# Kernel optimization log

Hardware: AMD Instinct MI355X
Metric: run time of the kernel (lower is better)

## Reference

```python
import jax, jax.numpy as jnp
import numpy as np

M, K = 8192, 4096
N_INT4, N_INT8 = 8192, 2816
N_TOTAL = N_INT4 + N_INT8


def setup_inputs() -> dict:
    key = jax.random.key(0)
    k1, k2, k3, k4, k5 = jax.random.split(key, 5)
    x = jax.random.normal(k1, (M, K), dtype=jnp.float32)
    # Precomputed dequantized weight buffers (what forward() actually consumes).
    # Scaled down ~1/sqrt(K) to keep activations O(1), mimicking dequantized int4/int8 weights.
    w_int4_deq = jax.random.normal(k2, (N_INT4, K), dtype=jnp.float32) * 0.02
    w_int8_deq = jax.random.normal(k3, (N_INT8, K), dtype=jnp.float32) * 0.02
    # inv_perm: random permutation mapping concatenated [int4|int8] channels back to original order
    inv_perm = jax.random.permutation(k4, N_TOTAL).astype(jnp.int64)
    bias = jax.random.normal(k5, (N_TOTAL,), dtype=jnp.float32)
    return {"x": x, "w_int4_deq": w_int4_deq, "w_int8_deq": w_int8_deq,
            "inv_perm": inv_perm, "bias": bias}


def reference(x, w_int4_deq, w_int8_deq, inv_perm, bias):
    # Two GEMMs on dequantized weight groups: y = x @ W^T
    y_int4 = jnp.einsum('mk,nk->mn', x, w_int4_deq)   # [M, N_int4]
    y_int8 = jnp.einsum('mk,nk->mn', x, w_int8_deq)   # [M, N_int8]
    y = jnp.concatenate([y_int4, y_int8], axis=-1)    # [M, N_total]
    # Output-channel permutation back to original layout, then bias add
    y = jnp.take(y, inv_perm, axis=-1) + bias
    return y
```

## Files before the change

kernel.cpp:

```cpp
#include <hip/hip_runtime.h>
#include <hip/hip_bf16.h>

#define M_DIM 8192
#define K_DIM 4096
#define N4    8192
#define N8    2816
#define NT    11008
#define TM    (M_DIM / 256)
#define TN    (NT / 256)
#define NKT   (K_DIM / 64)
#define NFULL 1280
#define GRID  1472

typedef __attribute__((ext_vector_type(4))) float  f32x4;
typedef __attribute__((ext_vector_type(4))) float  float4v;
typedef __attribute__((ext_vector_type(8))) __bf16 bf16x8;
typedef __attribute__((ext_vector_type(4))) unsigned short ushort4v;
typedef __attribute__((ext_vector_type(8))) unsigned short ushort8v;

__device__ __forceinline__ unsigned short f2bf(float f) {
  union { float f; unsigned int u; } v; v.f = f;
  unsigned int u = v.u;
  unsigned int r = u + 0x7FFFu + ((u >> 16) & 1u);
  return (unsigned short)(r >> 16);
}

__global__ void conv_x_kernel(const float* __restrict__ x,
                              unsigned short* __restrict__ xb, int n8) {
  int idx = blockIdx.x * blockDim.x + threadIdx.x;
  int stride = gridDim.x * blockDim.x;
  for (int i = idx; i < n8; i += stride) {
    const float4v* src = (const float4v*)(x + (size_t)i * 8);
    float4v a = src[0], b = src[1];
    ushort8v o;
    o[0] = f2bf(a[0]); o[1] = f2bf(a[1]); o[2] = f2bf(a[2]); o[3] = f2bf(a[3]);
    o[4] = f2bf(b[0]); o[5] = f2bf(b[1]); o[6] = f2bf(b[2]); o[7] = f2bf(b[3]);
    ((ushort8v*)xb)[i] = o;
  }
}

__global__ void conv_w_kernel(const float* __restrict__ w4,
                              const float* __restrict__ w8,
                              const int* __restrict__ inv_perm,
                              unsigned short* __restrict__ wb) {
  int j = blockIdx.x;
  int c = inv_perm[j];
  const float* src = (c < N4) ? (w4 + (size_t)c * K_DIM)
                              : (w8 + (size_t)(c - N4) * K_DIM);
  unsigned short* dst = wb + (size_t)j * K_DIM;
  int t = threadIdx.x;
#pragma unroll
  for (int it = 0; it < 4; ++it) {
    int e = it * 1024 + t * 4;
    float4v a = *(const float4v*)(src + e);
    ushort4v o;
    o[0] = f2bf(a[0]); o[1] = f2bf(a[1]); o[2] = f2bf(a[2]); o[3] = f2bf(a[3]);
    *(ushort4v*)(dst + e) = o;
  }
}

__global__ __launch_bounds__(512, 2)
void gemm256_kernel(const unsigned short* __restrict__ A,
                    const unsigned short* __restrict__ B,
                    const float* __restrict__ bias,
                    float* __restrict__ C) {
  __shared__ __align__(16) unsigned short lds[4 * 16384];

  int bid = blockIdx.x;
  int vbid, mhalf, is_half;
  if (bid < NFULL) { vbid = bid; mhalf = 0; is_half = 0; }
  else { int h = bid - NFULL; vbid = NFULL + (h >> 1); mhalf = h & 1; is_half = 1; }
  int wgid = (vbid & 7) * ((TM * TN) / 8) + (vbid >> 3);
  int tile_m = wgid / TN;
  int tile_n = wgid % TN;

  const int tid  = threadIdx.x;
  const int wid  = tid >> 6;
  const int lane = tid & 63;
  const int wr  = wid >> 2;
  const int wcn = wid & 3;
  const int l15 = lane & 15;
  const int rswz  = (lane & 7) << 4;
  const int coff0 = (((lane >> 4) * 16) + 0)  ^ rswz;
  const int coff1 = (((lane >> 4) * 16) + 64) ^ rswz;
  const int st_row8 = lane >> 3;
  const int st_scol = ((lane & 7) * 16) ^ ((lane & 0x38) << 1);

  const size_t brow0 = (size_t)tile_n * 256;

  auto stage = [&](const unsigned short* __restrict__ g, size_t grow0,
                   unsigned short* ltile, int q, int ktelem) {
    int row = q * 64 + wid * 8 + st_row8;
    const unsigned short* src =
        g + (grow0 + (size_t)row) * K_DIM + ktelem + (st_scol >> 1);
    unsigned short* dst = ltile + (q * 64 + wid * 8) * 64;
    __builtin_amdgcn_global_load_lds(
        (const __attribute__((address_space(1))) void*)src,
        (__attribute__((address_space(3))) void*)dst, 16, 0, 0);
  };
  auto fragld = [&](const unsigned short* ltile, int row, int coff) -> bf16x8 {
    return *(const bf16x8*)((const char*)ltile + row * 128 + coff);
  };

  if (is_half) {
    const size_t arowh = (size_t)tile_m * 256 + (size_t)mhalf * 128;
    f32x4 acch[4][4];
#pragma unroll
    for (int i = 0; i < 4; ++i)
#pragma unroll
      for (int j = 0; j < 4; ++j) acch[i][j] = (f32x4){0.f, 0.f, 0.f, 0.f};

    stage(A, arowh, lds + 0, 0, 0);      stage(A, arowh, lds + 0, 1, 0);
    stage(B, brow0, lds + 16384, 0, 0);  stage(B, brow0, lds + 16384, 1, 0);
    stage(B, brow0, lds + 16384, 2, 0);  stage(B, brow0, lds + 16384, 3, 0);
    asm volatile("s_waitcnt vmcnt(0)" ::: "memory");
    __builtin_amdgcn_s_barrier();

#pragma unroll 1
    for (int u = 0; u < NKT; ++u) {
      unsigned short* Ac = lds + (u & 1) * 32768;
      unsigned short* Bc = Ac + 16384;
      unsigned short* An = lds + (32768 - (u & 1) * 32768);
      if (u + 1 < NKT) {
        int kn = (u + 1) * 64;
        stage(A, arowh, An, 0, kn);      stage(A, arowh, An, 1, kn);
        stage(B, brow0, An + 16384, 0, kn); stage(B, brow0, An + 16384, 1, kn);
        stage(B, brow0, An + 16384, 2, kn); stage(B, brow0, An + 16384, 3, kn);
      }
      bf16x8 ah[4][2], bh[4][2];
#pragma unroll
      for (int m = 0; m < 4; ++m) {
        int row = wr * 64 + m * 16 + l15;
        ah[m][0] = fragld(Ac, row, coff0);
        ah[m][1] = fragld(Ac, row, coff1);
      }
#pragma unroll
      for (int n = 0; n < 4; ++n) {
        int row = wcn * 64 + n * 16 + l15;
        bh[n][0] = fragld(Bc, row, coff0);
        bh[n][1] = fragld(Bc, row, coff1);
      }
      asm volatile("s_waitcnt lgkmcnt(0)" ::: "memory");
      __builtin_amdgcn_sched_barrier(0);
      __builtin_amdgcn_s_setprio(1);
#pragma unroll
      for (int m = 0; m < 4; ++m)
#pragma unroll
        for (int n = 0; n < 4; ++n) {
          acch[m][n] = __builtin_amdgcn_mfma_f32_16x16x32_bf16(ah[m][0], bh[n][0], acch[m][n], 0, 0, 0);
          acch[m][n] = __builtin_amdgcn_mfma_f32_16x16x32_bf16(ah[m][1], bh[n][1], acch[m][n], 0, 0, 0);
        }
      __builtin_amdgcn_s_setprio(0);
      asm volatile("s_waitcnt vmcnt(0)" ::: "memory");
      __builtin_amdgcn_s_barrier();
    }

#pragma unroll
    for (int n = 0; n < 4; ++n) {
      int col = tile_n * 256 + wcn * 64 + n * 16 + l15;
      float bv = bias[col];
#pragma unroll
      for (int m = 0; m < 4; ++m) {
        int row0 = tile_m * 256 + mhalf * 128 + wr * 64 + m * 16 + ((lane >> 4) * 4);
#pragma unroll
        for (int r = 0; r < 4; ++r) {
          C[(size_t)(row0 + r) * NT + col] = acch[m][n][r] + bv;
        }
      }
    }
    return;
  }

  const size_t arow0 = (size_t)tile_m * 256;

  f32x4 acc[8][4];
#pragma unroll
  for (int i = 0; i < 8; ++i)
#pragma unroll
    for (int j = 0; j < 4; ++j) acc[i][j] = (f32x4){0.f, 0.f, 0.f, 0.f};

  bf16x8 b0[2][2];

  stage(A, arow0, lds + 0,     0, 0);  stage(A, arow0, lds + 0,     2, 0);
  stage(A, arow0, lds + 0,     1, 0);  stage(A, arow0, lds + 0,     3, 0);
  stage(B, brow0, lds + 16384, 0, 0);  stage(B, brow0, lds + 16384, 1, 0);
  stage(B, brow0, lds + 16384, 2, 0);  stage(B, brow0, lds + 16384, 3, 0);
  stage(A, arow0, lds + 32768, 0, 64); stage(A, arow0, lds + 32768, 2, 64);
  stage(B, brow0, lds + 49152, 0, 64); stage(B, brow0, lds + 49152, 1, 64);
  stage(B, brow0, lds + 49152, 2, 64); stage(B, brow0, lds + 49152, 3, 64);
  asm volatile("s_waitcnt vmcnt(6)" ::: "memory");
  __builtin_amdgcn_s_barrier();

#pragma unroll
  for (int n = 0; n < 2; ++n) {
    int row = wcn * 64 + n * 16 + l15;
    b0[n][0] = fragld(lds + 16384, row, coff0);
    b0[n][1] = fragld(lds + 16384, row, coff1);
  }

#define KITER(AC, BC, AN, UN1, UN2)                                           \
  {                                                                           \
    unsigned short* const Ac = (AC);                                          \
    unsigned short* const Bc = (BC);                                          \
    unsigned short* const An = (AN);                                          \
    const int un1 = (UN1);                                                    \
    const int un2 = (UN2);                                                    \
    bf16x8 a0[4][2], a1[4][2], b1[2][2];                                      \
                \
    _Pragma("unroll")                                                         \
    for (int m = 0; m < 4; ++m) {                                             \
      int row = wr * 128 + m * 16 + l15;                                      \
      a0[m][0] = fragld(Ac, row, coff0);                                      \
      a0[m][1] = fragld(Ac, row, coff1);                                      \
    }                                                                         \
    stage(A, arow0, An, 1, un1);                                              \
    stage(A, arow0, An, 3, un1);                                              \
    __builtin_amdgcn_s_barrier();                                             \
    asm volatile("s_waitcnt lgkmcnt(0)" ::: "memory");                        \
    __builtin_amdgcn_sched_barrier(0);                                        \
    __builtin_amdgcn_s_setprio(1);                                            \
    _Pragma("unroll")                                                         \
    for (int m = 0; m < 4; ++m)                                               \
      _Pragma("unroll")                                                       \
      for (int n = 0; n < 2; ++n) {                                           \
        acc[m][n] = __builtin_amdgcn_mfma_f32_16x16x32_bf16(a0[m][0], b0[n][0], acc[m][n], 0, 0, 0); \
        acc[m][n] = __builtin_amdgcn_mfma_f32_16x16x32_bf16(a0[m][1], b0[n][1], acc[m][n], 0, 0, 0); \
      }                                                                       \
    __builtin_amdgcn_s_setprio(0);                                            \
    __builtin_amdgcn_s_barrier();                                             \
     \
    _Pragma("unroll")                                                         \
    for (int n = 0; n < 2; ++n) {                                             \
      int row = wcn * 64 + (2 + n) * 16 + l15;                                \
      b1[n][0] = fragld(Bc, row, coff0);                                      \
      b1[n][1] = fragld(Bc, row, coff1);                                      \
    }                                                                         \
    stage(A, arow0, Ac, 0, un2);                                              \
    stage(A, arow0, Ac, 2, un2);                                              \
    __builtin_amdgcn_s_barrier();                                             \
    asm volatile("s_waitcnt lgkmcnt(0)" ::: "memory");                        \
    __builtin_amdgcn_sched_barrier(0);                                        \
    __builtin_amdgcn_s_setprio(1);                                            \
    _Pragma("unroll")                                                         \
    for (int m = 0; m < 4; ++m)                                               \
      _Pragma("unroll")                                                       \
      for (int n = 0; n < 2; ++n) {                                           \
        acc[m][2 + n] = __builtin_amdgcn_mfma_f32_16x16x32_bf16(a0[m][0], b1[n][0], acc[m][2 + n], 0, 0, 0); \
        acc[m][2 + n] = __builtin_amdgcn_mfma_f32_16x16x32_bf16(a0[m][1], b1[n][1], acc[m][2 + n], 0, 0, 0); \
      }                                                                       \
    __builtin_amdgcn_s_setprio(0);                                            \
    asm volatile("s_waitcnt vmcnt(10)" ::: "memory");      \
    __builtin_amdgcn_s_barrier();                                             \
            \
    _Pragma("unroll")                                                         \
    for (int m = 0; m < 4; ++m) {                                             \
      int row = wr * 128 + 64 + m * 16 + l15;                                 \
      a1[m][0] = fragld(Ac, row, coff0);                                      \
      a1[m][1] = fragld(Ac, row, coff1);                                      \
    }                                                                         \
    stage(B, brow0, Bc, 0, un2);                                              \
    stage(B, brow0, Bc, 1, un2);                                              \
    __builtin_amdgcn_s_barrier();                                             \
    asm volatile("s_waitcnt lgkmcnt(0)" ::: "memory");                        \
    __builtin_amdgcn_sched_barrier(0);                                        \
    __builtin_amdgcn_s_setprio(1);                                            \
    _Pragma("unroll")                                                         \
    for (int m = 0; m < 4; ++m)                                               \
      _Pragma("unroll")                                                       \
      for (int n = 0; n < 2; ++n) {                                           \
        acc[4 + m][n] = __builtin_amdgcn_mfma_f32_16x16x32_bf16(a1[m][0], b0[n][0], acc[4 + m][n], 0, 0, 0); \
        acc[4 + m][n] = __builtin_amdgcn_mfma_f32_16x16x32_bf16(a1[m][1], b0[n][1], acc[4 + m][n], 0, 0, 0); \
      }                                                                       \
    __builtin_amdgcn_s_setprio(0);                                            \
    __builtin_amdgcn_s_barrier();                                             \
                             \
    stage(B, brow0, Bc, 2, un2);                                              \
    stage(B, brow0, Bc, 3, un2);                                              \
    asm volatile("s_waitcnt vmcnt(8)" ::: "memory");                          \
    __builtin_amdgcn_s_barrier();                                             \
    _Pragma("unroll")                                                         \
    for (int n = 0; n < 2; ++n) {                                             \
      int row = wcn * 64 + n * 16 + l15;                                      \
      b0[n][0] = fragld(An + 16384, row, coff0);                              \
      b0[n][1] = fragld(An + 16384, row, coff1);                              \
    }                                                                         \
    __builtin_amdgcn_s_setprio(1);                                            \
    _Pragma("unroll")                                                         \
    for (int m = 0; m < 4; ++m)                                               \
      _Pragma("unroll")                                                       \
      for (int n = 0; n < 2; ++n) {                                           \
        acc[4 + m][2 + n] = __builtin_amdgcn_mfma_f32_16x16x32_bf16(a1[m][0], b1[n][0], acc[4 + m][2 + n], 0, 0, 0); \
        acc[4 + m][2 + n] = __builtin_amdgcn_mfma_f32_16x16x32_bf16(a1[m][1], b1[n][1], acc[4 + m][2 + n], 0, 0, 0); \
      }                                                                       \
    __builtin_amdgcn_s_setprio(0);                                            \
    __builtin_amdgcn_s_barrier();                                             \
  }

#pragma unroll 1
  for (int u = 0; u < NKT; u += 2) {
    const int k1 = ((u + 1 < NKT) ? (u + 1) : (NKT - 1)) * 64;
    const int k2 = ((u + 2 < NKT) ? (u + 2) : (NKT - 1)) * 64;
    const int k3 = ((u + 3 < NKT) ? (u + 3) : (NKT - 1)) * 64;
    KITER(lds + 0,     lds + 16384, lds + 32768, k1, k2);
    KITER(lds + 32768, lds + 49152, lds + 0,     k2, k3);
  }
#undef KITER

#pragma unroll
  for (int n = 0; n < 4; ++n) {
    int col = tile_n * 256 + wcn * 64 + n * 16 + l15;
    float bv = bias[col];
#pragma unroll
    for (int m = 0; m < 8; ++m) {
      int row0 = tile_m * 256 + wr * 128 + m * 16 + ((lane >> 4) * 4);
#pragma unroll
      for (int r = 0; r < 4; ++r) {
        C[(size_t)(row0 + r) * NT + col] = acc[m][n][r] + bv;
      }
    }
  }
}

__global__ void gemm_fused_f32_kernel(const float* __restrict__ x,
                                      const float* __restrict__ w4,
                                      const float* __restrict__ w8,
                                      const int* __restrict__ inv_perm,
                                      const float* __restrict__ bias,
                                      float* __restrict__ C) {
  __shared__ __align__(16) unsigned short Alds[128 * 64];
  __shared__ __align__(16) unsigned short Blds[128 * 64];

  int bid = blockIdx.x;
  int wgid = (bid & 7) * ((M_DIM / 128) * (NT / 128) / 8) + (bid >> 3);
  int tile_n = wgid % (NT / 128);
  int tile_m = wgid / (NT / 128);

  const int tid  = threadIdx.x;
  const int wid  = tid >> 6;
  const int lane = tid & 63;
  const int wr = wid >> 1, wc = wid & 1;

  f32x4 acc[4][4];
#pragma unroll
  for (int i = 0; i < 4; ++i)
#pragma unroll
    for (int j = 0; j < 4; ++j) acc[i][j] = (f32x4){0.f, 0.f, 0.f, 0.f};

  const int lrow = lane >> 3;
  const int lcol = (lane & 7) * 8;

  const float* asrc[4];
  const float* bsrc[4];
  int ldsoff[4];
#pragma unroll
  for (int s = 0; s < 4; ++s) {
    int rb = s * 32 + wid * 8 + lrow;
    asrc[s] = x + (size_t)(tile_m * 128 + rb) * K_DIM + lcol;
    int c = inv_perm[tile_n * 128 + rb];
    bsrc[s] = ((c < N4) ? (w4 + (size_t)c * K_DIM)
                        : (w8 + (size_t)(c - N4) * K_DIM)) + lcol;
    ldsoff[s] = rb * 64 + lcol;
  }

  for (int kt = 0; kt < K_DIM; kt += 64) {
#pragma unroll
    for (int s = 0; s < 4; ++s) {
      float4v a0 = *(const float4v*)(asrc[s] + kt);
      float4v a1 = *(const float4v*)(asrc[s] + kt + 4);
      float4v b0 = *(const float4v*)(bsrc[s] + kt);
      float4v b1 = *(const float4v*)(bsrc[s] + kt + 4);
      ushort8v oa, ob;
      oa[0]=f2bf(a0[0]); oa[1]=f2bf(a0[1]); oa[2]=f2bf(a0[2]); oa[3]=f2bf(a0[3]);
      oa[4]=f2bf(a1[0]); oa[5]=f2bf(a1[1]); oa[6]=f2bf(a1[2]); oa[7]=f2bf(a1[3]);
      ob[0]=f2bf(b0[0]); ob[1]=f2bf(b0[1]); ob[2]=f2bf(b0[2]); ob[3]=f2bf(b0[3]);
      ob[4]=f2bf(b1[0]); ob[5]=f2bf(b1[1]); ob[6]=f2bf(b1[2]); ob[7]=f2bf(b1[3]);
      *(ushort8v*)&Alds[ldsoff[s]] = oa;
      *(ushort8v*)&Blds[ldsoff[s]] = ob;
    }
    __syncthreads();

#pragma unroll
    for (int kk = 0; kk < 2; ++kk) {
      bf16x8 af[4], bfr[4];
#pragma unroll
      for (int i = 0; i < 4; ++i) {
        int row = wr * 64 + i * 16 + (lane & 15);
        af[i] = *(const bf16x8*)&Alds[row * 64 + kk * 32 + (lane >> 4) * 8];
      }
#pragma unroll
      for (int j = 0; j < 4; ++j) {
        int row = wc * 64 + j * 16 + (lane & 15);
        bfr[j] = *(const bf16x8*)&Blds[row * 64 + kk * 32 + (lane >> 4) * 8];
      }
#pragma unroll
      for (int i = 0; i < 4; ++i)
#pragma unroll
        for (int j = 0; j < 4; ++j)
          acc[i][j] = __builtin_amdgcn_mfma_f32_16x16x32_bf16(af[i], bfr[j], acc[i][j], 0, 0, 0);
    }
    __syncthreads();
  }

#pragma unroll
  for (int j = 0; j < 4; ++j) {
    int col = tile_n * 128 + wc * 64 + j * 16 + (lane & 15);
    float bv = bias[col];
#pragma unroll
    for (int i = 0; i < 4; ++i) {
      int row0 = tile_m * 128 + wr * 64 + i * 16 + ((lane >> 4) * 4);
#pragma unroll
      for (int r = 0; r < 4; ++r) {
        C[(size_t)(row0 + r) * NT + col] = acc[i][j][r] + bv;
      }
    }
  }
}

extern "C" void kernel_launch(void* const* d_in, const int* in_sizes, int n_in,
                              void* d_out, int out_size, void* d_ws, size_t ws_size,
                              hipStream_t stream) {
  const float* x    = (const float*)d_in[0];
  const float* w4   = (const float*)d_in[1];
  const float* w8   = (const float*)d_in[2];
  const int*   perm = (const int*)d_in[3];
  const float* bias = (const float*)d_in[4];
  float*       out  = (float*)d_out;

  const size_t xb_bytes = (size_t)M_DIM * K_DIM * 2;
  const size_t wb_bytes = (size_t)NT * K_DIM * 2;

  if (ws_size >= xb_bytes + wb_bytes) {
    unsigned short* xb = (unsigned short*)d_ws;
    unsigned short* wb = xb + (size_t)M_DIM * K_DIM;
    conv_x_kernel<<<2048, 256, 0, stream>>>(x, xb, (M_DIM * K_DIM) / 8);
    conv_w_kernel<<<NT, 256, 0, stream>>>(w4, w8, perm, wb);
    gemm256_kernel<<<GRID, 512, 0, stream>>>(xb, wb, bias, out);
  } else {
    int grid = (M_DIM / 128) * (NT / 128);
    gemm_fused_f32_kernel<<<grid, 256, 0, stream>>>(x, w4, w8, perm, bias, out);
  }
}
```

Measured before the change: 731.2 us.

## Pre-swizzle weights into MFMA fragment layout and load B directly to registers

The weight conversion kernel now writes bf16 weights in a per-wave MFMA fragment order, so the GEMM can load B fragments straight from global memory into registers instead of staging them through LDS. LDS usage is halved (only A is staged), and the main-loop pipeline is simplified to one A-tile prefetch per k-step with fewer barriers. The aim is to cut LDS traffic and barrier overhead and possibly raise occupancy. The cost is that B is re-read from global/L2 by each wave without LDS sharing, and global-load latency is exposed within the k-step.

```diff
diff --git a/kernel.cpp b/kernel.cpp
--- a/kernel.cpp
+++ b/kernel.cpp
@@ -39,32 +39,46 @@
   }
 }
 
-__global__ void conv_w_kernel(const float* __restrict__ w4,
-                              const float* __restrict__ w8,
-                              const int* __restrict__ inv_perm,
-                              unsigned short* __restrict__ wb) {
-  int j = blockIdx.x;
-  int c = inv_perm[j];
-  const float* src = (c < N4) ? (w4 + (size_t)c * K_DIM)
-                              : (w8 + (size_t)(c - N4) * K_DIM);
-  unsigned short* dst = wb + (size_t)j * K_DIM;
-  int t = threadIdx.x;
-#pragma unroll
-  for (int it = 0; it < 4; ++it) {
-    int e = it * 1024 + t * 4;
-    float4v a = *(const float4v*)(src + e);
-    ushort4v o;
-    o[0] = f2bf(a[0]); o[1] = f2bf(a[1]); o[2] = f2bf(a[2]); o[3] = f2bf(a[3]);
-    *(ushort4v*)(dst + e) = o;
+__global__ void conv_w2_kernel(const float* __restrict__ w4,
+                               const float* __restrict__ w8,
+                               const int* __restrict__ inv_perm,
+                               unsigned short* __restrict__ w2) {
+  int task = blockIdx.x * 4 + (threadIdx.x >> 6);
+  int lane = threadIdx.x & 63;
+  int rg = task >> 4;
+  int uq = task & 15;
+  int r  = rg * 16 + (lane & 15);
+  int u  = uq * 4 + (lane >> 4);
+  int pr = inv_perm[r];
+  const float* src = (pr < N4) ? (w4 + (size_t)pr * K_DIM)
+                               : (w8 + (size_t)(pr - N4) * K_DIM);
+  float4v v[16];
+#pragma unroll
+  for (int i = 0; i < 16; ++i) v[i] = *(const float4v*)(src + u * 64 + i * 4);
+
+  const int T = rg >> 2;
+  const int n = rg & 3;
+  const size_t cbase = (((size_t)T * 64 + u) * 8 + n * 2) * 64 + (lane & 15);
+#pragma unroll
+  for (int kk = 0; kk < 2; ++kk) {
+#pragma unroll
+    for (int g = 0; g < 4; ++g) {
+      float4v lo = v[kk * 8 + g * 2], hi = v[kk * 8 + g * 2 + 1];
+      ushort8v o;
+      o[0] = f2bf(lo[0]); o[1] = f2bf(lo[1]); o[2] = f2bf(lo[2]); o[3] = f2bf(lo[3]);
+      o[4] = f2bf(hi[0]); o[5] = f2bf(hi[1]); o[6] = f2bf(hi[2]); o[7] = f2bf(hi[3]);
+      size_t ci = cbase + (size_t)kk * 64 + (g << 4);
+      *(ushort8v*)(w2 + ci * 8) = o;
+    }
   }
 }
 
 __global__ __launch_bounds__(512, 2)
 void gemm256_kernel(const unsigned short* __restrict__ A,
-                    const unsigned short* __restrict__ B,
+                    const unsigned short* __restrict__ Bw2,
                     const float* __restrict__ bias,
                     float* __restrict__ C) {
-  __shared__ __align__(16) unsigned short lds[4 * 16384];
+  __shared__ __align__(16) unsigned short lds[2 * 16384];
 
   int bid = blockIdx.x;
   int vbid, mhalf, is_half;
@@ -85,60 +99,54 @@
   const int coff1 = (((lane >> 4) * 16) + 64) ^ rswz;
   const int st_row8 = lane >> 3;
   const int st_scol = ((lane & 7) * 16) ^ ((lane & 0x38) << 1);
-
-  const size_t brow0 = (size_t)tile_n * 256;
-
-  auto stage = [&](const unsigned short* __restrict__ g, size_t grow0,
+  const int dstoff  = wid * 512;
+
+  const unsigned short* w2lane =
+      Bw2 + ((size_t)(tile_n * 4 + wcn) * 32768 + (size_t)lane) * 8;
+
+  auto stage = [&](const unsigned short* __restrict__ srcb,
                    unsigned short* ltile, int q, int ktelem) {
-    int row = q * 64 + wid * 8 + st_row8;
-    const unsigned short* src =
-        g + (grow0 + (size_t)row) * K_DIM + ktelem + (st_scol >> 1);
-    unsigned short* dst = ltile + (q * 64 + wid * 8) * 64;
     __builtin_amdgcn_global_load_lds(
-        (const __attribute__((address_space(1))) void*)src,
-        (__attribute__((address_space(3))) void*)dst, 16, 0, 0);
+        (const __attribute__((address_space(1))) void*)(srcb + q * (64 * K_DIM) + ktelem),
+        (__attribute__((address_space(3))) void*)(ltile + q * 4096 + dstoff), 16, 0, 0);
   };
   auto fragld = [&](const unsigned short* ltile, int row, int coff) -> bf16x8 {
     return *(const bf16x8*)((const char*)ltile + row * 128 + coff);
   };
 
   if (is_half) {
-    const size_t arowh = (size_t)tile_m * 256 + (size_t)mhalf * 128;
+    const unsigned short* aSh =
+        A + ((size_t)tile_m * 256 + (size_t)mhalf * 128 + (size_t)(wid * 8 + st_row8)) * K_DIM
+          + (st_scol >> 1);
     f32x4 acch[4][4];
 #pragma unroll
     for (int i = 0; i < 4; ++i)
 #pragma unroll
       for (int j = 0; j < 4; ++j) acch[i][j] = (f32x4){0.f, 0.f, 0.f, 0.f};
 
-    stage(A, arowh, lds + 0, 0, 0);      stage(A, arowh, lds + 0, 1, 0);
-    stage(B, brow0, lds + 16384, 0, 0);  stage(B, brow0, lds + 16384, 1, 0);
-    stage(B, brow0, lds + 16384, 2, 0);  stage(B, brow0, lds + 16384, 3, 0);
+    stage(aSh, lds + 0, 0, 0); stage(aSh, lds + 0, 1, 0);
     asm volatile("s_waitcnt vmcnt(0)" ::: "memory");
     __builtin_amdgcn_s_barrier();
 
 #pragma unroll 1
     for (int u = 0; u < NKT; ++u) {
-      unsigned short* Ac = lds + (u & 1) * 32768;
-      unsigned short* Bc = Ac + 16384;
-      unsigned short* An = lds + (32768 - (u & 1) * 32768);
-      if (u + 1 < NKT) {
-        int kn = (u + 1) * 64;
-        stage(A, arowh, An, 0, kn);      stage(A, arowh, An, 1, kn);
-        stage(B, brow0, An + 16384, 0, kn); stage(B, brow0, An + 16384, 1, kn);
-        stage(B, brow0, An + 16384, 2, kn); stage(B, brow0, An + 16384, 3, kn);
-      }
-      bf16x8 ah[4][2], bh[4][2];
+      unsigned short* Ac = lds + (u & 1) * 8192;
+      unsigned short* An = lds + (8192 - (u & 1) * 8192);
+      const unsigned short* wB = w2lane + (size_t)u * 4096;
+      bf16x8 bh[4][2];
+#pragma unroll
+      for (int n = 0; n < 4; ++n) {
+        bh[n][0] = *(const bf16x8*)(wB + (n * 2) * 512);
+        bh[n][1] = *(const bf16x8*)(wB + (n * 2 + 1) * 512);
+      }
+      int kn = ((u + 1 < NKT) ? (u + 1) : (NKT - 1)) * 64;
+      stage(aSh, An, 0, kn); stage(aSh, An, 1, kn);
+      bf16x8 ah[4][2];
 #pragma unroll
       for (int m = 0; m < 4; ++m) {
         int row = wr * 64 + m * 16 + l15;
         ah[m][0] = fragld(Ac, row, coff0);
         ah[m][1] = fragld(Ac, row, coff1);
-      }
-#pragma unroll
-      for (int n = 0; n < 4; ++n) {
-        int row = wcn * 64 + n * 16 + l15;
-        bh[n][0] = fragld(Bc, row, coff0);
-        bh[n][1] = fragld(Bc, row, coff1);
       }
       asm volatile("s_waitcnt lgkmcnt(0)" ::: "memory");
       __builtin_amdgcn_sched_barrier(0);
@@ -171,7 +179,8 @@
     return;
   }
 
-  const size_t arow0 = (size_t)tile_m * 256;
+  const unsigned short* aS =
+      A + ((size_t)tile_m * 256 + (size_t)(wid * 8 + st_row8)) * K_DIM + (st_scol >> 1);
 
   f32x4 acc[8][4];
 #pragma unroll
@@ -179,132 +188,72 @@
 #pragma unroll
     for (int j = 0; j < 4; ++j) acc[i][j] = (f32x4){0.f, 0.f, 0.f, 0.f};
 
-  bf16x8 b0[2][2];
-
-  stage(A, arow0, lds + 0,     0, 0);  stage(A, arow0, lds + 0,     2, 0);
-  stage(A, arow0, lds + 0,     1, 0);  stage(A, arow0, lds + 0,     3, 0);
-  stage(B, brow0, lds + 16384, 0, 0);  stage(B, brow0, lds + 16384, 1, 0);
-  stage(B, brow0, lds + 16384, 2, 0);  stage(B, brow0, lds + 16384, 3, 0);
-  stage(A, arow0, lds + 32768, 0, 64); stage(A, arow0, lds + 32768, 2, 64);
-  stage(B, brow0, lds + 49152, 0, 64); stage(B, brow0, lds + 49152, 1, 64);
-  stage(B, brow0, lds + 49152, 2, 64); stage(B, brow0, lds + 49152, 3, 64);
-  asm volatile("s_waitcnt vmcnt(6)" ::: "memory");
+  stage(aS, lds + 0, 0, 0); stage(aS, lds + 0, 1, 0);
+  stage(aS, lds + 0, 2, 0); stage(aS, lds + 0, 3, 0);
+  asm volatile("s_waitcnt vmcnt(0)" ::: "memory");
   __builtin_amdgcn_s_barrier();
 
-#pragma unroll
-  for (int n = 0; n < 2; ++n) {
-    int row = wcn * 64 + n * 16 + l15;
-    b0[n][0] = fragld(lds + 16384, row, coff0);
-    b0[n][1] = fragld(lds + 16384, row, coff1);
-  }
-
-#define KITER(AC, BC, AN, UN1, UN2)                                           \
+#define CLUSTER(MB, AF)                                                       \
+    _Pragma("unroll")                                                         \
+    for (int m = 0; m < 4; ++m)                                               \
+      _Pragma("unroll")                                                       \
+      for (int n = 0; n < 4; ++n) {                                           \
+        acc[(MB)+m][n] = __builtin_amdgcn_mfma_f32_16x16x32_bf16(AF[m][0], bh[n][0], acc[(MB)+m][n], 0, 0, 0); \
+        acc[(MB)+m][n] = __builtin_amdgcn_mfma_f32_16x16x32_bf16(AF[m][1], bh[n][1], acc[(MB)+m][n], 0, 0, 0); \
+      }
+
+#define KITER(AC, AN, UB, KN1E)                                               \
   {                                                                           \
     unsigned short* const Ac = (AC);                                          \
-    unsigned short* const Bc = (BC);                                          \
     unsigned short* const An = (AN);                                          \
-    const int un1 = (UN1);                                                    \
-    const int un2 = (UN2);                                                    \
-    bf16x8 a0[4][2], a1[4][2], b1[2][2];                                      \
-                \
+    const unsigned short* wB = w2lane + (size_t)(UB) * 4096;                  \
+    bf16x8 bh[4][2];                                                          \
+    _Pragma("unroll")                                                         \
+    for (int n = 0; n < 4; ++n) {                                             \
+      bh[n][0] = *(const bf16x8*)(wB + (n * 2) * 512);                        \
+      bh[n][1] = *(const bf16x8*)(wB + (n * 2 + 1) * 512);                    \
+    }                                                                         \
+    bf16x8 a0[4][2], a1[4][2];                                                \
     _Pragma("unroll")                                                         \
     for (int m = 0; m < 4; ++m) {                                             \
       int row = wr * 128 + m * 16 + l15;                                      \
       a0[m][0] = fragld(Ac, row, coff0);                                      \
       a0[m][1] = fragld(Ac, row, coff1);                                      \
     }                                                                         \
-    stage(A, arow0, An, 1, un1);                                              \
-    stage(A, arow0, An, 3, un1);                                              \
-    __builtin_amdgcn_s_barrier();                                             \
-    asm volatile("s_waitcnt lgkmcnt(0)" ::: "memory");                        \
     __builtin_amdgcn_sched_barrier(0);                                        \
-    __builtin_amdgcn_s_setprio(1);                                            \
-    _Pragma("unroll")                                                         \
-    for (int m = 0; m < 4; ++m)                                               \
-      _Pragma("unroll")                                                       \
-      for (int n = 0; n < 2; ++n) {                                           \
-        acc[m][n] = __builtin_amdgcn_mfma_f32_16x16x32_bf16(a0[m][0], b0[n][0], acc[m][n], 0, 0, 0); \
-        acc[m][n] = __builtin_amdgcn_mfma_f32_16x16x32_bf16(a0[m][1], b0[n][1], acc[m][n], 0, 0, 0); \
-      }                                                                       \
-    __builtin_amdgcn_s_setprio(0);                                            \
-    __builtin_amdgcn_s_barrier();                                             \
-     \
-    _Pragma("unroll")                                                         \
-    for (int n = 0; n < 2; ++n) {                                             \
-      int row = wcn * 64 + (2 + n) * 16 + l15;                                \
-      b1[n][0] = fragld(Bc, row, coff0);                                      \
-      b1[n][1] = fragld(Bc, row, coff1);                                      \
-    }                                                                         \
-    stage(A, arow0, Ac, 0, un2);                                              \
-    stage(A, arow0, Ac, 2, un2);                                              \
-    __builtin_amdgcn_s_barrier();                                             \
-    asm volatile("s_waitcnt lgkmcnt(0)" ::: "memory");                        \
-    __builtin_amdgcn_sched_barrier(0);                                        \
-    __builtin_amdgcn_s_setprio(1);                                            \
-    _Pragma("unroll")                                                         \
-    for (int m = 0; m < 4; ++m)                                               \
-      _Pragma("unroll")                                                       \
-      for (int n = 0; n < 2; ++n) {                                           \
-        acc[m][2 + n] = __builtin_amdgcn_mfma_f32_16x16x32_bf16(a0[m][0], b1[n][0], acc[m][2 + n], 0, 0, 0); \
-        acc[m][2 + n] = __builtin_amdgcn_mfma_f32_16x16x32_bf16(a0[m][1], b1[n][1], acc[m][2 + n], 0, 0, 0); \
-      }                                                                       \
-    __builtin_amdgcn_s_setprio(0);                                            \
-    asm volatile("s_waitcnt vmcnt(10)" ::: "memory");      \
-    __builtin_amdgcn_s_barrier();                                             \
-            \
     _Pragma("unroll")                                                         \
     for (int m = 0; m < 4; ++m) {                                             \
       int row = wr * 128 + 64 + m * 16 + l15;                                 \
       a1[m][0] = fragld(Ac, row, coff0);                                      \
       a1[m][1] = fragld(Ac, row, coff1);                                      \
     }                                                                         \
-    stage(B, brow0, Bc, 0, un2);                                              \
-    stage(B, brow0, Bc, 1, un2);                                              \
-    __builtin_amdgcn_s_barrier();                                             \
-    asm volatile("s_waitcnt lgkmcnt(0)" ::: "memory");                        \
+    stage(aS, An, 0, (KN1E));                                                 \
+    stage(aS, An, 1, (KN1E));                                                 \
+    stage(aS, An, 2, (KN1E));                                                 \
+    stage(aS, An, 3, (KN1E));                                                 \
+    asm volatile("s_waitcnt lgkmcnt(8)" ::: "memory");           \
     __builtin_amdgcn_sched_barrier(0);                                        \
     __builtin_amdgcn_s_setprio(1);                                            \
-    _Pragma("unroll")                                                         \
-    for (int m = 0; m < 4; ++m)                                               \
-      _Pragma("unroll")                                                       \
-      for (int n = 0; n < 2; ++n) {                                           \
-        acc[4 + m][n] = __builtin_amdgcn_mfma_f32_16x16x32_bf16(a1[m][0], b0[n][0], acc[4 + m][n], 0, 0, 0); \
-        acc[4 + m][n] = __builtin_amdgcn_mfma_f32_16x16x32_bf16(a1[m][1], b0[n][1], acc[4 + m][n], 0, 0, 0); \
-      }                                                                       \
+    CLUSTER(0, a0)                                                            \
     __builtin_amdgcn_s_setprio(0);                                            \
-    __builtin_amdgcn_s_barrier();                                             \
-                             \
-    stage(B, brow0, Bc, 2, un2);                                              \
-    stage(B, brow0, Bc, 3, un2);                                              \
-    asm volatile("s_waitcnt vmcnt(8)" ::: "memory");                          \
-    __builtin_amdgcn_s_barrier();                                             \
-    _Pragma("unroll")                                                         \
-    for (int n = 0; n < 2; ++n) {                                             \
-      int row = wcn * 64 + n * 16 + l15;                                      \
-      b0[n][0] = fragld(An + 16384, row, coff0);                              \
-      b0[n][1] = fragld(An + 16384, row, coff1);                              \
-    }                                                                         \
+    asm volatile("s_waitcnt lgkmcnt(0)" ::: "memory");           \
+    __builtin_amdgcn_sched_barrier(0);                                        \
     __builtin_amdgcn_s_setprio(1);                                            \
-    _Pragma("unroll")                                                         \
-    for (int m = 0; m < 4; ++m)                                               \
-      _Pragma("unroll")                                                       \
-      for (int n = 0; n < 2; ++n) {                                           \
-        acc[4 + m][2 + n] = __builtin_amdgcn_mfma_f32_16x16x32_bf16(a1[m][0], b1[n][0], acc[4 + m][2 + n], 0, 0, 0); \
-        acc[4 + m][2 + n] = __builtin_amdgcn_mfma_f32_16x16x32_bf16(a1[m][1], b1[n][1], acc[4 + m][2 + n], 0, 0, 0); \
-      }                                                                       \
+    CLUSTER(4, a1)                                                            \
     __builtin_amdgcn_s_setprio(0);                                            \
+    asm volatile("s_waitcnt vmcnt(0)" ::: "memory");    \
     __builtin_amdgcn_s_barrier();                                             \
   }
 
 #pragma unroll 1
   for (int u = 0; u < NKT; u += 2) {
-    const int k1 = ((u + 1 < NKT) ? (u + 1) : (NKT - 1)) * 64;
-    const int k2 = ((u + 2 < NKT) ? (u + 2) : (NKT - 1)) * 64;
-    const int k3 = ((u + 3 < NKT) ? (u + 3) : (NKT - 1)) * 64;
-    KITER(lds + 0,     lds + 16384, lds + 32768, k1, k2);
-    KITER(lds + 32768, lds + 49152, lds + 0,     k2, k3);
+    const int k1 = (u + 1 < NKT) ? (u + 1) : (NKT - 1);
+    const int k2 = (u + 2 < NKT) ? (u + 2) : (NKT - 1);
+    KITER(lds + 0,     lds + 16384, u,     k1 * 64);
+    KITER(lds + 16384, lds + 0,     u + 1, k2 * 64);
   }
 #undef KITER
+#undef CLUSTER
 
 #pragma unroll
   for (int n = 0; n < 4; ++n) {
@@ -431,10 +380,10 @@
 
   if (ws_size >= xb_bytes + wb_bytes) {
     unsigned short* xb = (unsigned short*)d_ws;
-    unsigned short* wb = xb + (size_t)M_DIM * K_DIM;
+    unsigned short* w2 = xb + (size_t)M_DIM * K_DIM;
     conv_x_kernel<<<2048, 256, 0, stream>>>(x, xb, (M_DIM * K_DIM) / 8);
-    conv_w_kernel<<<NT, 256, 0, stream>>>(w4, w8, perm, wb);
-    gemm256_kernel<<<GRID, 512, 0, stream>>>(xb, wb, bias, out);
+    conv_w2_kernel<<<2752, 256, 0, stream>>>(w4, w8, perm, w2);
+    gemm256_kernel<<<GRID, 512, 0, stream>>>(xb, w2, bias, out);
   } else {
     int grid = (M_DIM / 128) * (NT / 128);
     gemm_fused_f32_kernel<<<grid, 256, 0, stream>>>(x, w4, w8, perm, bias, out);
```

New measurement: 953.5 us. 30.4% more time.
